# Kernel tuning notes

Hardware: AMD Instinct MI355X
Metric: run time of the kernel (lower is better)

The kernel has to match this reference:

```python
import jax, jax.numpy as jnp
import numpy as np

HIDDEN = 2048
INTERMEDIATE = 8192
NUM_EXPERTS = 8
VOCAB = 100000
EXPERT_INTER = INTERMEDIATE // NUM_EXPERTS  # 1024
B, S = 4, 4096


def setup_inputs() -> dict:
    key = jax.random.key(0)
    k1, k2, k3, k4, k5 = jax.random.split(key, 5)
    hidden_states = jax.random.normal(k1, (B, S, HIDDEN), dtype=jnp.float32)
    token_ids = jax.random.randint(k2, (B, S), 0, VOCAB, dtype=jnp.int64)
    scale = 0.02
    gate_proj = jax.random.normal(k3, (NUM_EXPERTS, HIDDEN, EXPERT_INTER), dtype=jnp.float32) * scale
    up_proj = jax.random.normal(k4, (NUM_EXPERTS, HIDDEN, EXPERT_INTER), dtype=jnp.float32) * scale
    down_proj = jax.random.normal(k5, (NUM_EXPERTS, EXPERT_INTER, HIDDEN), dtype=jnp.float32) * scale
    return {
        "hidden_states": hidden_states,
        "token_ids": token_ids,
        "gate_proj": gate_proj,
        "up_proj": up_proj,
        "down_proj": down_proj,
    }


def _token_to_expert(token_ids):
    # Buffer in the torch module maps contiguous vocab buckets to experts;
    # remainder tokens go to the last expert.
    tokens_per_expert = VOCAB // NUM_EXPERTS
    ids = jnp.clip(token_ids, 0, VOCAB - 1)
    return jnp.minimum(ids // tokens_per_expert, NUM_EXPERTS - 1)


def reference(hidden_states, token_ids, gate_proj, up_proj, down_proj):
    batch, seq_len, hidden = hidden_states.shape
    expert_ids = _token_to_expert(token_ids).reshape(-1)  # [T]
    x = hidden_states.reshape(-1, hidden)  # [T, H]
    out = jnp.zeros_like(x)
    # Fixed small loop over experts (structurally distinct weight slices).
    # Masked dense compute is mathematically identical to the torch module's
    # sort -> per-expert GEMM -> scatter-back (the permutation cancels).
    for e in range(NUM_EXPERTS):
        mask = (expert_ids == e)[:, None]  # [T, 1]
        g = x @ gate_proj[e]               # [T, I_e]
        u = x @ up_proj[e]                 # [T, I_e]
        y = (jax.nn.silu(g) * u) @ down_proj[e]  # [T, H]
        out = out + jnp.where(mask, y, jnp.zeros((), dtype=y.dtype))
    return out.reshape(batch, seq_len, hidden)
```

## Files before the change

### kernel.cpp

```cpp
#include <hip/hip_runtime.h>
#include <hip/hip_bf16.h>
#include <cstdint>
#include <cstddef>

#define HIDDEN   2048
#define EINTER   1024
#define NEXP     8
#define VOCAB_SZ 100000
#define TOK_PER_EXP (VOCAB_SZ / NEXP)

typedef unsigned short u16;
typedef __attribute__((ext_vector_type(8))) short short8;
typedef __attribute__((ext_vector_type(4))) float floatx4;

__device__ __forceinline__ int expert_of(int id) {
  id = id < 0 ? 0 : (id > VOCAB_SZ - 1 ? VOCAB_SZ - 1 : id);
  int e = id / TOK_PER_EXP;
  return e > NEXP - 1 ? NEXP - 1 : e;
}

__device__ __forceinline__ void gl16(const u16* g, u16* l) {
  __builtin_amdgcn_global_load_lds(
      (const __attribute__((address_space(1))) uint32_t*)g,
      (__attribute__((address_space(3))) uint32_t*)l, 16, 0, 0);
}

__device__ __forceinline__ short8 ldfrag(const u16* base, int row, int chunk) {
  return *(const short8*)(base + (row << 6) + (((chunk ^ (row & 7))) << 3));
}

__global__ void count_kernel(const int* __restrict__ tok_ids, int* __restrict__ counts, int T) {
  int t = blockIdx.x * blockDim.x + threadIdx.x;
  if (t < T) atomicAdd(&counts[expert_of(tok_ids[t])], 1);
}

__global__ void scan_kernel(const int* __restrict__ counts, int* __restrict__ offsets,
                            int* __restrict__ cursors) {
  if (threadIdx.x == 0) {
    int s = 0;
    for (int e = 0; e < NEXP; ++e) { offsets[e] = s; cursors[e] = s; s += counts[e]; }
  }
}

__global__ void scatter_kernel(const int* __restrict__ tok_ids, int* __restrict__ cursors,
                               int* __restrict__ tok_list, int T) {
  int t = blockIdx.x * blockDim.x + threadIdx.x;
  if (t < T) {
    int e = expert_of(tok_ids[t]);
    int pos = atomicAdd(&cursors[e], 1);
    tok_list[pos] = t;
  }
}

__global__ void gather_x_kernel(const float* __restrict__ x, const int* __restrict__ tok_list,
                                u16* __restrict__ xp) {
  const int row = blockIdx.x;
  const int tok = tok_list[row];
  const float* src = x + (size_t)tok * HIDDEN;
  u16* dst = xp + (size_t)row * HIDDEN;
  const int k = threadIdx.x * 8;
  float4 a = *(const float4*)(src + k);
  float4 b = *(const float4*)(src + k + 4);
  union { uint4 u; u16 s[8]; } pk;
  const float f[8] = {a.x, a.y, a.z, a.w, b.x, b.y, b.z, b.w};
#pragma unroll
  for (int i = 0; i < 8; ++i) {
    __hip_bfloat16 h = __float2bfloat16(f[i]);
    pk.s[i] = *reinterpret_cast<u16*>(&h);
  }
  *(uint4*)(dst + k) = pk.u;
}

__global__ void transpose_cvt64(const float* __restrict__ in0, u16* __restrict__ out0,
                                const float* __restrict__ in1, u16* __restrict__ out1,
                                int R, int C, int split) {
  __shared__ float ts[64][65];
  const int z = blockIdx.z;
  const bool first = (z < split) || (in1 == nullptr);
  const float* in = first ? in0 : in1;
  u16* outp = first ? out0 : out1;
  const int e = first ? z : z - split;
  const size_t bo = (size_t)e * R * C;
  const int c0 = blockIdx.x * 64, r0 = blockIdx.y * 64;
  const int lr = threadIdx.x >> 2, lq = threadIdx.x & 3;
#pragma unroll
  for (int j = 0; j < 4; ++j)
    *(float4*)&ts[lr][lq * 16 + j * 4] =
        *(const float4*)&in[bo + (size_t)(r0 + lr) * C + c0 + lq * 16 + j * 4];
  __syncthreads();
#pragma unroll
  for (int j = 0; j < 2; ++j) {
    union { uint4 u; u16 s[8]; } pk;
#pragma unroll
    for (int i = 0; i < 8; ++i) {
      __hip_bfloat16 h = __float2bfloat16(ts[lq * 16 + j * 8 + i][lr]);
      pk.s[i] = *reinterpret_cast<u16*>(&h);
    }
    *(uint4*)&outp[bo + (size_t)(c0 + lr) * R + r0 + lq * 16 + j * 8] = pk.u;
  }
}

__global__ __launch_bounds__(256, 2) void gate_up_mfma(
    const u16* __restrict__ xp, const u16* __restrict__ Gt, const u16* __restrict__ Ut,
    const int* __restrict__ counts, const int* __restrict__ offsets,
    u16* __restrict__ act) {
  __shared__ __align__(16) u16 As[128 * 64];
  __shared__ __align__(16) u16 Bg[64 * 64];
  __shared__ __align__(16) u16 Bu[64 * 64];

  const int e = blockIdx.z;
  const int cnt = counts[e];
  const int row0 = blockIdx.y * 128;
  if (row0 >= cnt) return;
  const int off = offsets[e];
  const int i0 = blockIdx.x * 64;

  const int tid  = threadIdx.x;
  const int lane = tid & 63;
  const int wave = tid >> 6;
  const int quad = lane >> 4;
  const int l16  = lane & 15;

  const int lrow   = lane >> 3;
  const int lchunk = (lane & 7) ^ lrow;

  const int wrow = (wave & 1) * 64;
  const int wcol = (wave >> 1) * 32;

  const u16* aptr[4];
#pragma unroll
  for (int it = 0; it < 4; ++it) {
    int r = ((wave + 4 * it) << 3) + lrow;
    int rg = row0 + r; rg = rg < cnt ? rg : cnt - 1;
    aptr[it] = xp + (size_t)(off + rg) * HIDDEN + (lchunk << 3);
  }
  const u16* gptr[2];
  const u16* uptr[2];
#pragma unroll
  for (int it = 0; it < 2; ++it) {
    int n = ((wave + 4 * it) << 3) + lrow;
    gptr[it] = Gt + ((size_t)e * EINTER + i0 + n) * HIDDEN + (lchunk << 3);
    uptr[it] = Ut + ((size_t)e * EINTER + i0 + n) * HIDDEN + (lchunk << 3);
  }

  floatx4 accg[4][2], accu[4][2];
#pragma unroll
  for (int mf = 0; mf < 4; ++mf)
#pragma unroll
    for (int nf = 0; nf < 2; ++nf) {
      floatx4 z = {0.f, 0.f, 0.f, 0.f};
      accg[mf][nf] = z; accu[mf][nf] = z;
    }

  for (int k0 = 0; k0 < HIDDEN; k0 += 64) {
#pragma unroll
    for (int it = 0; it < 4; ++it)
      gl16(aptr[it] + k0, &As[(wave + 4 * it) << 9]);
#pragma unroll
    for (int it = 0; it < 2; ++it) {
      gl16(gptr[it] + k0, &Bg[(wave + 4 * it) << 9]);
      gl16(uptr[it] + k0, &Bu[(wave + 4 * it) << 9]);
    }
    __syncthreads();
#pragma unroll
    for (int s = 0; s < 2; ++s) {
      short8 af[4], bgf[2], buf2[2];
#pragma unroll
      for (int mf = 0; mf < 4; ++mf)
        af[mf] = ldfrag(As, wrow + mf * 16 + l16, s * 4 + quad);
#pragma unroll
      for (int nf = 0; nf < 2; ++nf) {
        bgf[nf]  = ldfrag(Bg, wcol + nf * 16 + l16, s * 4 + quad);
        buf2[nf] = ldfrag(Bu, wcol + nf * 16 + l16, s * 4 + quad);
      }
#pragma unroll
      for (int mf = 0; mf < 4; ++mf)
#pragma unroll
        for (int nf = 0; nf < 2; ++nf) {
          accg[mf][nf] = __builtin_amdgcn_mfma_f32_16x16x32_bf16(af[mf], bgf[nf],  accg[mf][nf], 0, 0, 0);
          accu[mf][nf] = __builtin_amdgcn_mfma_f32_16x16x32_bf16(af[mf], buf2[nf], accu[mf][nf], 0, 0, 0);
        }
    }
    __syncthreads();
  }

#pragma unroll
  for (int mf = 0; mf < 4; ++mf)
#pragma unroll
    for (int nf = 0; nf < 2; ++nf)
#pragma unroll
      for (int rg = 0; rg < 4; ++rg) {
        int r = wrow + mf * 16 + quad * 4 + rg;
        if (row0 + r < cnt) {
          float g = accg[mf][nf][rg];
          float u = accu[mf][nf][rg];
          float y = (g / (1.f + __expf(-g))) * u;
          __hip_bfloat16 h = __float2bfloat16(y);
          act[((size_t)(off + row0 + r)) * EINTER + i0 + wcol + nf * 16 + l16] =
              *reinterpret_cast<u16*>(&h);
        }
      }
}

__global__ __launch_bounds__(256, 2) void down_mfma(
    const u16* __restrict__ act, const u16* __restrict__ Dt,
    const int* __restrict__ counts, const int* __restrict__ offsets,
    const int* __restrict__ tok_list, float* __restrict__ out) {
  __shared__ __align__(16) u16 As[128 * 64];
  __shared__ __align__(16) u16 Bs[128 * 64];
  __shared__ int toks[128];

  const int e = blockIdx.z;
  const int cnt = counts[e];
  const int row0 = blockIdx.y * 128;
  if (row0 >= cnt) return;
  const int off = offsets[e];
  const int j0 = blockIdx.x * 128;

  const int tid  = threadIdx.x;
  const int lane = tid & 63;
  const int wave = tid >> 6;
  const int quad = lane >> 4;
  const int l16  = lane & 15;

  const int lrow   = lane >> 3;
  const int lchunk = (lane & 7) ^ lrow;

  const int wrow = (wave & 1) * 64;
  const int wcol = (wave >> 1) * 64;

  if (tid < 128) {
    int r = row0 + tid;
    toks[tid] = tok_list[off + (r < cnt ? r : cnt - 1)];
  }

  const u16* aptr[4];
  const u16* dptr[4];
#pragma unroll
  for (int it = 0; it < 4; ++it) {
    int r = ((wave + 4 * it) << 3) + lrow;
    int rg = row0 + r; rg = rg < cnt ? rg : cnt - 1;
    aptr[it] = act + (size_t)(off + rg) * EINTER + (lchunk << 3);
    dptr[it] = Dt + ((size_t)e * HIDDEN + j0 + r) * EINTER + (lchunk << 3);
  }

  floatx4 acc[4][4];
#pragma unroll
  for (int mf = 0; mf < 4; ++mf)
#pragma unroll
    for (int nf = 0; nf < 4; ++nf) {
      floatx4 z = {0.f, 0.f, 0.f, 0.f};
      acc[mf][nf] = z;
    }

  for (int k0 = 0; k0 < EINTER; k0 += 64) {
#pragma unroll
    for (int it = 0; it < 4; ++it) {
      gl16(aptr[it] + k0, &As[(wave + 4 * it) << 9]);
      gl16(dptr[it] + k0, &Bs[(wave + 4 * it) << 9]);
    }
    __syncthreads();
#pragma unroll
    for (int s = 0; s < 2; ++s) {
      short8 af[4], bf[4];
#pragma unroll
      for (int mf = 0; mf < 4; ++mf)
        af[mf] = ldfrag(As, wrow + mf * 16 + l16, s * 4 + quad);
#pragma unroll
      for (int nf = 0; nf < 4; ++nf)
        bf[nf] = ldfrag(Bs, wcol + nf * 16 + l16, s * 4 + quad);
#pragma unroll
      for (int mf = 0; mf < 4; ++mf)
#pragma unroll
        for (int nf = 0; nf < 4; ++nf)
          acc[mf][nf] = __builtin_amdgcn_mfma_f32_16x16x32_bf16(af[mf], bf[nf], acc[mf][nf], 0, 0, 0);
    }
    __syncthreads();
  }

#pragma unroll
  for (int mf = 0; mf < 4; ++mf)
#pragma unroll
    for (int nf = 0; nf < 4; ++nf)
#pragma unroll
      for (int rg = 0; rg < 4; ++rg) {
        int r = wrow + mf * 16 + quad * 4 + rg;
        if (row0 + r < cnt)
          out[(size_t)toks[r] * HIDDEN + j0 + wcol + nf * 16 + l16] = acc[mf][nf][rg];
      }
}

#define TM 64
#define TN 64
#define TK 16

__global__ __launch_bounds__(256, 2) void gate_up_fp32(
    const float* __restrict__ x, const float* __restrict__ G, const float* __restrict__ U,
    const int* __restrict__ counts, const int* __restrict__ offsets,
    const int* __restrict__ tok_list, float* __restrict__ act) {
  __shared__ __align__(16) float Xs[TK][TM + 4];
  __shared__ __align__(16) float Gs[TK][TN];
  __shared__ __align__(16) float Us[TK][TN];
  __shared__ int toks[TM];
  const int e = blockIdx.z, cnt = counts[e], row0 = blockIdx.y * TM;
  if (row0 >= cnt) return;
  const int off = offsets[e], i0 = blockIdx.x * TN, tid = threadIdx.x;
  if (tid < TM) { int r = row0 + tid; toks[tid] = tok_list[off + (r < cnt ? r : 0)]; }
  __syncthreads();
  const float* Ge = G + (size_t)e * HIDDEN * EINTER + i0;
  const float* Ue = U + (size_t)e * HIDDEN * EINTER + i0;
  const int kk_ld = tid & 15, r_ld = tid >> 4, i_ld = tid & 63, k_ld = tid >> 6;
  const int tx = tid & 15, ty = tid >> 4;
  float ag[4][4] = {{0.f}}, au[4][4] = {{0.f}};
  for (int k0 = 0; k0 < HIDDEN; k0 += TK) {
#pragma unroll
    for (int rr = 0; rr < 4; ++rr) {
      int r = r_ld + rr * 16;
      Xs[kk_ld][r] = x[(size_t)toks[r] * HIDDEN + k0 + kk_ld];
    }
#pragma unroll
    for (int kk = 0; kk < 4; ++kk) {
      int k = k_ld + kk * 4;
      Gs[k][i_ld] = Ge[(size_t)(k0 + k) * EINTER + i_ld];
      Us[k][i_ld] = Ue[(size_t)(k0 + k) * EINTER + i_ld];
    }
    __syncthreads();
#pragma unroll
    for (int kk = 0; kk < TK; ++kk) {
      float4 a = *(const float4*)&Xs[kk][ty * 4];
      float4 bg = *(const float4*)&Gs[kk][tx * 4];
      float4 bu = *(const float4*)&Us[kk][tx * 4];
      const float av[4] = {a.x, a.y, a.z, a.w}, bgv[4] = {bg.x, bg.y, bg.z, bg.w},
                  buv[4] = {bu.x, bu.y, bu.z, bu.w};
#pragma unroll
      for (int i = 0; i < 4; ++i)
#pragma unroll
        for (int j = 0; j < 4; ++j) {
          ag[i][j] = fmaf(av[i], bgv[j], ag[i][j]);
          au[i][j] = fmaf(av[i], buv[j], au[i][j]);
        }
    }
    __syncthreads();
  }
#pragma unroll
  for (int i = 0; i < 4; ++i) {
    int r = row0 + ty * 4 + i;
    if (r < cnt) {
      float4 o; float* op = (float*)&o;
#pragma unroll
      for (int j = 0; j < 4; ++j) {
        float g = ag[i][j], u = au[i][j];
        op[j] = (g / (1.0f + expf(-g))) * u;
      }
      *(float4*)&act[(size_t)(off + r) * EINTER + i0 + tx * 4] = o;
    }
  }
}

__global__ __launch_bounds__(256, 2) void down_fp32(
    const float* __restrict__ act, const float* __restrict__ D,
    const int* __restrict__ counts, const int* __restrict__ offsets,
    const int* __restrict__ tok_list, float* __restrict__ out) {
  __shared__ __align__(16) float As[TK][TM + 4];
  __shared__ __align__(16) float Ds[TK][TN];
  __shared__ int toks[TM];
  const int e = blockIdx.z, cnt = counts[e], row0 = blockIdx.y * TM;
  if (row0 >= cnt) return;
  const int off = offsets[e], j0 = blockIdx.x * TN, tid = threadIdx.x;
  if (tid < TM) { int r = row0 + tid; toks[tid] = tok_list[off + (r < cnt ? r : 0)]; }
  const float* De = D + (size_t)e * EINTER * HIDDEN + j0;
  const int kk_ld = tid & 15, r_ld = tid >> 4, i_ld = tid & 63, k_ld = tid >> 6;
  const int tx = tid & 15, ty = tid >> 4;
  float acc[4][4] = {{0.f}};
  for (int k0 = 0; k0 < EINTER; k0 += TK) {
#pragma unroll
    for (int rr = 0; rr < 4; ++rr) {
      int r = r_ld + rr * 16;
      int grow = row0 + r;
      As[kk_ld][r] = act[(size_t)(off + (grow < cnt ? grow : 0)) * EINTER + k0 + kk_ld];
    }
#pragma unroll
    for (int kk = 0; kk < 4; ++kk) {
      int k = k_ld + kk * 4;
      Ds[k][i_ld] = De[(size_t)(k0 + k) * HIDDEN + i_ld];
    }
    __syncthreads();
#pragma unroll
    for (int kk = 0; kk < TK; ++kk) {
      float4 a = *(const float4*)&As[kk][ty * 4];
      float4 b = *(const float4*)&Ds[kk][tx * 4];
      const float av[4] = {a.x, a.y, a.z, a.w}, bv[4] = {b.x, b.y, b.z, b.w};
#pragma unroll
      for (int i = 0; i < 4; ++i)
#pragma unroll
        for (int j = 0; j < 4; ++j)
          acc[i][j] = fmaf(av[i], bv[j], acc[i][j]);
    }
    __syncthreads();
  }
#pragma unroll
  for (int i = 0; i < 4; ++i) {
    int r = row0 + ty * 4 + i;
    if (r < cnt) {
      float4 o = {acc[i][0], acc[i][1], acc[i][2], acc[i][3]};
      *(float4*)&out[(size_t)toks[ty * 4 + i] * HIDDEN + j0 + tx * 4] = o;
    }
  }
}

extern "C" void kernel_launch(void* const* d_in, const int* in_sizes, int n_in,
                              void* d_out, int out_size, void* d_ws, size_t ws_size,
                              hipStream_t stream) {
  const float* x       = (const float*)d_in[0];
  const int*   tok_ids = (const int*)d_in[1];
  const float* G       = (const float*)d_in[2];
  const float* U       = (const float*)d_in[3];
  const float* D       = (const float*)d_in[4];
  float* out = (float*)d_out;

  const int T = in_sizes[0] / HIDDEN;

  int* counts   = (int*)d_ws;
  int* offsets  = counts + NEXP;
  int* cursors  = offsets + NEXP;
  int* tok_list = cursors + NEXP;
  size_t hdr_bytes = (((size_t)(3 * NEXP + T) * sizeof(int)) + 255) & ~(size_t)255;

  hipMemsetAsync(counts, 0, NEXP * sizeof(int), stream);
  count_kernel<<<(T + 255) / 256, 256, 0, stream>>>(tok_ids, counts, T);
  scan_kernel<<<1, 64, 0, stream>>>(counts, offsets, cursors);
  scatter_kernel<<<(T + 255) / 256, 256, 0, stream>>>(tok_ids, cursors, tok_list, T);

  const size_t xp_bytes  = (size_t)T * HIDDEN * 2;
  const size_t w_bytes   = (size_t)NEXP * HIDDEN * EINTER * 2;
  const size_t act_bf16  = (size_t)T * EINTER * 2;
  const size_t need_bf16 = hdr_bytes + xp_bytes + 3 * w_bytes + act_bf16;

  if (ws_size >= need_bf16) {
    char* p = (char*)d_ws + hdr_bytes;
    u16* xp = (u16*)p;   p += xp_bytes;
    u16* Gt = (u16*)p;   p += w_bytes;
    u16* Ut = (u16*)p;   p += w_bytes;
    u16* Dt = (u16*)p;   p += w_bytes;
    u16* act = (u16*)p;

    gather_x_kernel<<<T, 256, 0, stream>>>(x, tok_list, xp);
    transpose_cvt64<<<dim3(EINTER / 64, HIDDEN / 64, 2 * NEXP), 256, 0, stream>>>(
        G, Gt, U, Ut, HIDDEN, EINTER, NEXP);
    transpose_cvt64<<<dim3(HIDDEN / 64, EINTER / 64, NEXP), 256, 0, stream>>>(
        D, Dt, nullptr, nullptr, EINTER, HIDDEN, NEXP);

    dim3 g1(EINTER / 64, (T + 127) / 128, NEXP);
    gate_up_mfma<<<g1, 256, 0, stream>>>(xp, Gt, Ut, counts, offsets, act);
    dim3 g2(HIDDEN / 128, (T + 127) / 128, NEXP);
    down_mfma<<<g2, 256, 0, stream>>>(act, Dt, counts, offsets, tok_list, out);
  } else {
    float* act = (float*)((char*)d_ws + hdr_bytes);
    dim3 g1(EINTER / TN, (T + TM - 1) / TM, NEXP);
    gate_up_fp32<<<g1, 256, 0, stream>>>(x, G, U, counts, offsets, tok_list, act);
    dim3 g2(HIDDEN / TN, (T + TM - 1) / TM, NEXP);
    down_fp32<<<g2, 256, 0, stream>>>(act, D, counts, offsets, tok_list, out);
  }
}
```

Baseline: 746.3 us.

## Rewrite MoE GEMMs as 8-wave double-buffered phased pipelines with larger tiles

Replaces the gate/up and down MFMA kernels with 512-thread versions that use 256-row tiles and wider column tiles. Shared memory is double-buffered, and each K step is split into four phases. In each phase, global-to-LDS loads for the next tile are interleaved with MFMA bursts, using explicit waitcnt, barriers and setprio. The aim is to hide global load latency and raise arithmetic intensity per block. The cost is much larger LDS use, which lowers occupancy, and more partially filled tiles per expert because the row granularity is coarser.

```diff
diff --git a/kernel.cpp b/kernel.cpp
--- a/kernel.cpp
+++ b/kernel.cpp
@@ -100,194 +100,371 @@
   }
 }
 
-__global__ __launch_bounds__(256, 2) void gate_up_mfma(
+
+__global__ __launch_bounds__(512, 2) void gate_up_8ph(
     const u16* __restrict__ xp, const u16* __restrict__ Gt, const u16* __restrict__ Ut,
     const int* __restrict__ counts, const int* __restrict__ offsets,
     u16* __restrict__ act) {
-  __shared__ __align__(16) u16 As[128 * 64];
-  __shared__ __align__(16) u16 Bg[64 * 64];
-  __shared__ __align__(16) u16 Bu[64 * 64];
+  __shared__ __align__(16) u16 As[2][256 * 64];
+  __shared__ __align__(16) u16 Bg[2][128 * 64];
+  __shared__ __align__(16) u16 Bu[2][128 * 64];
 
   const int e = blockIdx.z;
   const int cnt = counts[e];
-  const int row0 = blockIdx.y * 128;
+  const int row0 = blockIdx.y * 256;
   if (row0 >= cnt) return;
   const int off = offsets[e];
-  const int i0 = blockIdx.x * 64;
+  const int i0 = blockIdx.x * 128;
 
   const int tid  = threadIdx.x;
   const int lane = tid & 63;
-  const int wave = tid >> 6;
+  const int w    = tid >> 6;
+  const int wr   = w >> 2;
+  const int wc   = w & 3;
   const int quad = lane >> 4;
   const int l16  = lane & 15;
-
   const int lrow   = lane >> 3;
   const int lchunk = (lane & 7) ^ lrow;
 
-  const int wrow = (wave & 1) * 64;
-  const int wcol = (wave >> 1) * 32;
-
-  const u16* aptr[4];
-#pragma unroll
-  for (int it = 0; it < 4; ++it) {
-    int r = ((wave + 4 * it) << 3) + lrow;
-    int rg = row0 + r; rg = rg < cnt ? rg : cnt - 1;
-    aptr[it] = xp + (size_t)(off + rg) * HIDDEN + (lchunk << 3);
-  }
-  const u16* gptr[2];
-  const u16* uptr[2];
+  const u16* apt[4]; int abase[4];
+  {
+    const int bsel[4] = {w, w + 16, w + 8, w + 24};
+#pragma unroll
+    for (int i = 0; i < 4; ++i) {
+      int batch = bsel[i];
+      int r = batch * 8 + lrow;
+      int rg = row0 + r; rg = rg < cnt ? rg : cnt - 1;
+      apt[i] = xp + (size_t)(off + rg) * HIDDEN + (lchunk << 3);
+      abase[i] = batch << 9;
+    }
+  }
+  const u16 *gpt[2], *upt[2]; int bbase[2];
 #pragma unroll
   for (int it = 0; it < 2; ++it) {
-    int n = ((wave + 4 * it) << 3) + lrow;
-    gptr[it] = Gt + ((size_t)e * EINTER + i0 + n) * HIDDEN + (lchunk << 3);
-    uptr[it] = Ut + ((size_t)e * EINTER + i0 + n) * HIDDEN + (lchunk << 3);
-  }
-
-  floatx4 accg[4][2], accu[4][2];
-#pragma unroll
-  for (int mf = 0; mf < 4; ++mf)
-#pragma unroll
-    for (int nf = 0; nf < 2; ++nf) {
-      floatx4 z = {0.f, 0.f, 0.f, 0.f};
-      accg[mf][nf] = z; accu[mf][nf] = z;
-    }
-
-  for (int k0 = 0; k0 < HIDDEN; k0 += 64) {
-#pragma unroll
-    for (int it = 0; it < 4; ++it)
-      gl16(aptr[it] + k0, &As[(wave + 4 * it) << 9]);
-#pragma unroll
-    for (int it = 0; it < 2; ++it) {
-      gl16(gptr[it] + k0, &Bg[(wave + 4 * it) << 9]);
-      gl16(uptr[it] + k0, &Bu[(wave + 4 * it) << 9]);
-    }
-    __syncthreads();
-#pragma unroll
-    for (int s = 0; s < 2; ++s) {
-      short8 af[4], bgf[2], buf2[2];
-#pragma unroll
-      for (int mf = 0; mf < 4; ++mf)
-        af[mf] = ldfrag(As, wrow + mf * 16 + l16, s * 4 + quad);
+    int batch = w + 8 * it;
+    int n = batch * 8 + lrow;
+    gpt[it] = Gt + ((size_t)e * EINTER + i0 + n) * HIDDEN + (lchunk << 3);
+    upt[it] = Ut + ((size_t)e * EINTER + i0 + n) * HIDDEN + (lchunk << 3);
+    bbase[it] = batch << 9;
+  }
+
+  floatx4 accg[2][4][2], accu[2][4][2];
+#pragma unroll
+  for (int mh = 0; mh < 2; ++mh)
+#pragma unroll
+    for (int mf = 0; mf < 4; ++mf)
 #pragma unroll
       for (int nf = 0; nf < 2; ++nf) {
-        bgf[nf]  = ldfrag(Bg, wcol + nf * 16 + l16, s * 4 + quad);
-        buf2[nf] = ldfrag(Bu, wcol + nf * 16 + l16, s * 4 + quad);
+        floatx4 z = {0.f, 0.f, 0.f, 0.f};
+        accg[mh][mf][nf] = z; accu[mh][mf][nf] = z;
       }
-#pragma unroll
-      for (int mf = 0; mf < 4; ++mf)
-#pragma unroll
-        for (int nf = 0; nf < 2; ++nf) {
-          accg[mf][nf] = __builtin_amdgcn_mfma_f32_16x16x32_bf16(af[mf], bgf[nf],  accg[mf][nf], 0, 0, 0);
-          accu[mf][nf] = __builtin_amdgcn_mfma_f32_16x16x32_bf16(af[mf], buf2[nf], accu[mf][nf], 0, 0, 0);
+
+  gl16(apt[0], As[0] + abase[0]); gl16(apt[1], As[0] + abase[1]);
+  gl16(gpt[0], Bg[0] + bbase[0]); gl16(gpt[1], Bg[0] + bbase[1]);
+  gl16(upt[0], Bu[0] + bbase[0]); gl16(upt[1], Bu[0] + bbase[1]);
+  gl16(apt[2], As[0] + abase[2]); gl16(apt[3], As[0] + abase[3]);
+  asm volatile("s_waitcnt vmcnt(4)" ::: "memory");
+  __builtin_amdgcn_s_barrier();
+
+  const int NT = HIDDEN / 64;
+  for (int t = 0; t < NT; ++t) {
+    const int b  = t & 1;
+    const int kn = (t + 1 < NT) ? (t + 1) * 64 : 0;
+    const u16* Ar = As[b]; const u16* Gr = Bg[b]; const u16* Ur = Bu[b];
+    u16* Aw = As[b ^ 1];   u16* Gw = Bg[b ^ 1];   u16* Uw = Bu[b ^ 1];
+
+    short8 af[4][2], bg[2][2], bu[2][2];
+
+#pragma unroll
+    for (int mf = 0; mf < 4; ++mf)
+#pragma unroll
+      for (int s = 0; s < 2; ++s)
+        af[mf][s] = ldfrag(Ar, wr * 128 + mf * 16 + l16, s * 4 + quad);
+#pragma unroll
+    for (int nf = 0; nf < 2; ++nf)
+#pragma unroll
+      for (int s = 0; s < 2; ++s)
+        bg[nf][s] = ldfrag(Gr, wc * 32 + nf * 16 + l16, s * 4 + quad);
+    gl16(apt[0] + kn, Aw + abase[0]); gl16(apt[1] + kn, Aw + abase[1]);
+    gl16(gpt[0] + kn, Gw + bbase[0]); gl16(gpt[1] + kn, Gw + bbase[1]);
+    asm volatile("s_waitcnt vmcnt(6)" ::: "memory");
+    __builtin_amdgcn_s_barrier();
+    asm volatile("s_waitcnt lgkmcnt(0)" ::: "memory");
+    __builtin_amdgcn_sched_barrier(0);
+    __builtin_amdgcn_s_setprio(1);
+#pragma unroll
+    for (int s = 0; s < 2; ++s)
+#pragma unroll
+      for (int mf = 0; mf < 4; ++mf)
+#pragma unroll
+        for (int nf = 0; nf < 2; ++nf)
+          accg[0][mf][nf] = __builtin_amdgcn_mfma_f32_16x16x32_bf16(af[mf][s], bg[nf][s], accg[0][mf][nf], 0, 0, 0);
+    __builtin_amdgcn_s_setprio(0);
+    __builtin_amdgcn_sched_barrier(0);
+    __builtin_amdgcn_s_barrier();
+
+#pragma unroll
+    for (int nf = 0; nf < 2; ++nf)
+#pragma unroll
+      for (int s = 0; s < 2; ++s)
+        bu[nf][s] = ldfrag(Ur, wc * 32 + nf * 16 + l16, s * 4 + quad);
+    gl16(upt[0] + kn, Uw + bbase[0]); gl16(upt[1] + kn, Uw + bbase[1]);
+    asm volatile("s_waitcnt vmcnt(6)" ::: "memory");
+    __builtin_amdgcn_s_barrier();
+    asm volatile("s_waitcnt lgkmcnt(0)" ::: "memory");
+    __builtin_amdgcn_sched_barrier(0);
+    __builtin_amdgcn_s_setprio(1);
+#pragma unroll
+    for (int s = 0; s < 2; ++s)
+#pragma unroll
+      for (int mf = 0; mf < 4; ++mf)
+#pragma unroll
+        for (int nf = 0; nf < 2; ++nf)
+          accu[0][mf][nf] = __builtin_amdgcn_mfma_f32_16x16x32_bf16(af[mf][s], bu[nf][s], accu[0][mf][nf], 0, 0, 0);
+    __builtin_amdgcn_s_setprio(0);
+    __builtin_amdgcn_sched_barrier(0);
+    __builtin_amdgcn_s_barrier();
+
+#pragma unroll
+    for (int mf = 0; mf < 4; ++mf)
+#pragma unroll
+      for (int s = 0; s < 2; ++s)
+        af[mf][s] = ldfrag(Ar, wr * 128 + 64 + mf * 16 + l16, s * 4 + quad);
+    gl16(apt[2] + kn, Aw + abase[2]); gl16(apt[3] + kn, Aw + abase[3]);
+    __builtin_amdgcn_s_barrier();
+    asm volatile("s_waitcnt lgkmcnt(0)" ::: "memory");
+    __builtin_amdgcn_sched_barrier(0);
+    __builtin_amdgcn_s_setprio(1);
+#pragma unroll
+    for (int s = 0; s < 2; ++s)
+#pragma unroll
+      for (int mf = 0; mf < 4; ++mf)
+#pragma unroll
+        for (int nf = 0; nf < 2; ++nf)
+          accg[1][mf][nf] = __builtin_amdgcn_mfma_f32_16x16x32_bf16(af[mf][s], bg[nf][s], accg[1][mf][nf], 0, 0, 0);
+    __builtin_amdgcn_s_setprio(0);
+    __builtin_amdgcn_sched_barrier(0);
+    __builtin_amdgcn_s_barrier();
+
+    asm volatile("s_waitcnt vmcnt(4)" ::: "memory");
+    __builtin_amdgcn_s_barrier();
+    __builtin_amdgcn_s_setprio(1);
+#pragma unroll
+    for (int s = 0; s < 2; ++s)
+#pragma unroll
+      for (int mf = 0; mf < 4; ++mf)
+#pragma unroll
+        for (int nf = 0; nf < 2; ++nf)
+          accu[1][mf][nf] = __builtin_amdgcn_mfma_f32_16x16x32_bf16(af[mf][s], bu[nf][s], accu[1][mf][nf], 0, 0, 0);
+    __builtin_amdgcn_s_setprio(0);
+    __builtin_amdgcn_sched_barrier(0);
+    __builtin_amdgcn_s_barrier();
+  }
+  asm volatile("s_waitcnt vmcnt(0)" ::: "memory");
+
+#pragma unroll
+  for (int mh = 0; mh < 2; ++mh)
+#pragma unroll
+    for (int mf = 0; mf < 4; ++mf)
+#pragma unroll
+      for (int nf = 0; nf < 2; ++nf)
+#pragma unroll
+        for (int rg = 0; rg < 4; ++rg) {
+          int r = wr * 128 + mh * 64 + mf * 16 + quad * 4 + rg;
+          if (row0 + r < cnt) {
+            float g = accg[mh][mf][nf][rg];
+            float u = accu[mh][mf][nf][rg];
+            float y = (g / (1.f + __expf(-g))) * u;
+            __hip_bfloat16 h = __float2bfloat16(y);
+            act[((size_t)(off + row0 + r)) * EINTER + i0 + wc * 32 + nf * 16 + l16] =
+                *reinterpret_cast<u16*>(&h);
+          }
         }
-    }
-    __syncthreads();
-  }
-
-#pragma unroll
-  for (int mf = 0; mf < 4; ++mf)
-#pragma unroll
-    for (int nf = 0; nf < 2; ++nf)
-#pragma unroll
-      for (int rg = 0; rg < 4; ++rg) {
-        int r = wrow + mf * 16 + quad * 4 + rg;
-        if (row0 + r < cnt) {
-          float g = accg[mf][nf][rg];
-          float u = accu[mf][nf][rg];
-          float y = (g / (1.f + __expf(-g))) * u;
-          __hip_bfloat16 h = __float2bfloat16(y);
-          act[((size_t)(off + row0 + r)) * EINTER + i0 + wcol + nf * 16 + l16] =
-              *reinterpret_cast<u16*>(&h);
-        }
-      }
-}
-
-__global__ __launch_bounds__(256, 2) void down_mfma(
+}
+
+__global__ __launch_bounds__(512, 2) void down_8ph(
     const u16* __restrict__ act, const u16* __restrict__ Dt,
     const int* __restrict__ counts, const int* __restrict__ offsets,
     const int* __restrict__ tok_list, float* __restrict__ out) {
-  __shared__ __align__(16) u16 As[128 * 64];
-  __shared__ __align__(16) u16 Bs[128 * 64];
-  __shared__ int toks[128];
+  __shared__ __align__(16) u16 As[2][256 * 64];
+  __shared__ __align__(16) u16 Bs[2][256 * 64];
+  __shared__ int toks[256];
 
   const int e = blockIdx.z;
   const int cnt = counts[e];
-  const int row0 = blockIdx.y * 128;
+  const int row0 = blockIdx.y * 256;
   if (row0 >= cnt) return;
   const int off = offsets[e];
-  const int j0 = blockIdx.x * 128;
+  const int j0 = blockIdx.x * 256;
 
   const int tid  = threadIdx.x;
   const int lane = tid & 63;
-  const int wave = tid >> 6;
+  const int w    = tid >> 6;
+  const int wr   = w >> 2;
+  const int wc   = w & 3;
   const int quad = lane >> 4;
   const int l16  = lane & 15;
-
   const int lrow   = lane >> 3;
   const int lchunk = (lane & 7) ^ lrow;
 
-  const int wrow = (wave & 1) * 64;
-  const int wcol = (wave >> 1) * 64;
-
-  if (tid < 128) {
+  if (tid < 256) {
     int r = row0 + tid;
     toks[tid] = tok_list[off + (r < cnt ? r : cnt - 1)];
   }
 
-  const u16* aptr[4];
-  const u16* dptr[4];
-#pragma unroll
-  for (int it = 0; it < 4; ++it) {
-    int r = ((wave + 4 * it) << 3) + lrow;
-    int rg = row0 + r; rg = rg < cnt ? rg : cnt - 1;
-    aptr[it] = act + (size_t)(off + rg) * EINTER + (lchunk << 3);
-    dptr[it] = Dt + ((size_t)e * HIDDEN + j0 + r) * EINTER + (lchunk << 3);
-  }
-
-  floatx4 acc[4][4];
-#pragma unroll
-  for (int mf = 0; mf < 4; ++mf)
-#pragma unroll
-    for (int nf = 0; nf < 4; ++nf) {
-      floatx4 z = {0.f, 0.f, 0.f, 0.f};
-      acc[mf][nf] = z;
-    }
-
-  for (int k0 = 0; k0 < EINTER; k0 += 64) {
-#pragma unroll
-    for (int it = 0; it < 4; ++it) {
-      gl16(aptr[it] + k0, &As[(wave + 4 * it) << 9]);
-      gl16(dptr[it] + k0, &Bs[(wave + 4 * it) << 9]);
-    }
-    __syncthreads();
-#pragma unroll
-    for (int s = 0; s < 2; ++s) {
-      short8 af[4], bf[4];
-#pragma unroll
-      for (int mf = 0; mf < 4; ++mf)
-        af[mf] = ldfrag(As, wrow + mf * 16 + l16, s * 4 + quad);
-#pragma unroll
-      for (int nf = 0; nf < 4; ++nf)
-        bf[nf] = ldfrag(Bs, wcol + nf * 16 + l16, s * 4 + quad);
-#pragma unroll
-      for (int mf = 0; mf < 4; ++mf)
-#pragma unroll
-        for (int nf = 0; nf < 4; ++nf)
-          acc[mf][nf] = __builtin_amdgcn_mfma_f32_16x16x32_bf16(af[mf], bf[nf], acc[mf][nf], 0, 0, 0);
-    }
-    __syncthreads();
-  }
-
-#pragma unroll
-  for (int mf = 0; mf < 4; ++mf)
-#pragma unroll
-    for (int nf = 0; nf < 4; ++nf)
-#pragma unroll
-      for (int rg = 0; rg < 4; ++rg) {
-        int r = wrow + mf * 16 + quad * 4 + rg;
-        if (row0 + r < cnt)
-          out[(size_t)toks[r] * HIDDEN + j0 + wcol + nf * 16 + l16] = acc[mf][nf][rg];
-      }
+  const u16* apt[4]; int abase[4];
+  {
+    const int bsel[4] = {w, w + 16, w + 8, w + 24};
+#pragma unroll
+    for (int i = 0; i < 4; ++i) {
+      int batch = bsel[i];
+      int r = batch * 8 + lrow;
+      int rg = row0 + r; rg = rg < cnt ? rg : cnt - 1;
+      apt[i] = act + (size_t)(off + rg) * EINTER + (lchunk << 3);
+      abase[i] = batch << 9;
+    }
+  }
+  const u16* dpt[4]; int dbase[4];
+#pragma unroll
+  for (int i = 0; i < 4; ++i) {
+    int batch = w + 8 * i;
+    int n = j0 + batch * 8 + lrow;
+    dpt[i] = Dt + ((size_t)e * HIDDEN + n) * EINTER + (lchunk << 3);
+    dbase[i] = batch << 9;
+  }
+
+  floatx4 acc[2][2][4][2];
+#pragma unroll
+  for (int mh = 0; mh < 2; ++mh)
+#pragma unroll
+    for (int nh = 0; nh < 2; ++nh)
+#pragma unroll
+      for (int mf = 0; mf < 4; ++mf)
+#pragma unroll
+        for (int nf = 0; nf < 2; ++nf) {
+          floatx4 z = {0.f, 0.f, 0.f, 0.f};
+          acc[mh][nh][mf][nf] = z;
+        }
+
+  asm volatile("s_waitcnt lgkmcnt(0)" ::: "memory");
+  gl16(apt[0], As[0] + abase[0]); gl16(apt[1], As[0] + abase[1]);
+  gl16(dpt[0], Bs[0] + dbase[0]); gl16(dpt[1], Bs[0] + dbase[1]);
+  gl16(dpt[2], Bs[0] + dbase[2]); gl16(dpt[3], Bs[0] + dbase[3]);
+  gl16(apt[2], As[0] + abase[2]); gl16(apt[3], As[0] + abase[3]);
+  asm volatile("s_waitcnt vmcnt(4)" ::: "memory");
+  __builtin_amdgcn_s_barrier();
+
+  const int NT = EINTER / 64;
+  for (int t = 0; t < NT; ++t) {
+    const int b  = t & 1;
+    const int kn = (t + 1 < NT) ? (t + 1) * 64 : 0;
+    const u16* Ar = As[b]; const u16* Br = Bs[b];
+    u16* Aw = As[b ^ 1];   u16* Bw = Bs[b ^ 1];
+
+    short8 af[4][2], b0[2][2], b1[2][2];
+
+#pragma unroll
+    for (int mf = 0; mf < 4; ++mf)
+#pragma unroll
+      for (int s = 0; s < 2; ++s)
+        af[mf][s] = ldfrag(Ar, wr * 128 + mf * 16 + l16, s * 4 + quad);
+#pragma unroll
+    for (int nf = 0; nf < 2; ++nf)
+#pragma unroll
+      for (int s = 0; s < 2; ++s)
+        b0[nf][s] = ldfrag(Br, wc * 32 + nf * 16 + l16, s * 4 + quad);
+    gl16(apt[0] + kn, Aw + abase[0]); gl16(apt[1] + kn, Aw + abase[1]);
+    gl16(dpt[0] + kn, Bw + dbase[0]); gl16(dpt[1] + kn, Bw + dbase[1]);
+    asm volatile("s_waitcnt vmcnt(6)" ::: "memory");
+    __builtin_amdgcn_s_barrier();
+    asm volatile("s_waitcnt lgkmcnt(0)" ::: "memory");
+    __builtin_amdgcn_sched_barrier(0);
+    __builtin_amdgcn_s_setprio(1);
+#pragma unroll
+    for (int s = 0; s < 2; ++s)
+#pragma unroll
+      for (int mf = 0; mf < 4; ++mf)
+#pragma unroll
+        for (int nf = 0; nf < 2; ++nf)
+          acc[0][0][mf][nf] = __builtin_amdgcn_mfma_f32_16x16x32_bf16(af[mf][s], b0[nf][s], acc[0][0][mf][nf], 0, 0, 0);
+    __builtin_amdgcn_s_setprio(0);
+    __builtin_amdgcn_sched_barrier(0);
+    __builtin_amdgcn_s_barrier();
+
+#pragma unroll
+    for (int nf = 0; nf < 2; ++nf)
+#pragma unroll
+      for (int s = 0; s < 2; ++s)
+        b1[nf][s] = ldfrag(Br, 128 + wc * 32 + nf * 16 + l16, s * 4 + quad);
+    gl16(dpt[2] + kn, Bw + dbase[2]); gl16(dpt[3] + kn, Bw + dbase[3]);
+    asm volatile("s_waitcnt vmcnt(6)" ::: "memory");
+    __builtin_amdgcn_s_barrier();
+    asm volatile("s_waitcnt lgkmcnt(0)" ::: "memory");
+    __builtin_amdgcn_sched_barrier(0);
+    __builtin_amdgcn_s_setprio(1);
+#pragma unroll
+    for (int s = 0; s < 2; ++s)
+#pragma unroll
+      for (int mf = 0; mf < 4; ++mf)
+#pragma unroll
+        for (int nf = 0; nf < 2; ++nf)
+          acc[0][1][mf][nf] = __builtin_amdgcn_mfma_f32_16x16x32_bf16(af[mf][s], b1[nf][s], acc[0][1][mf][nf], 0, 0, 0);
+    __builtin_amdgcn_s_setprio(0);
+    __builtin_amdgcn_sched_barrier(0);
+    __builtin_amdgcn_s_barrier();
+
+#pragma unroll
+    for (int mf = 0; mf < 4; ++mf)
+#pragma unroll
+      for (int s = 0; s < 2; ++s)
+        af[mf][s] = ldfrag(Ar, wr * 128 + 64 + mf * 16 + l16, s * 4 + quad);
+    gl16(apt[2] + kn, Aw + abase[2]); gl16(apt[3] + kn, Aw + abase[3]);
+    __builtin_amdgcn_s_barrier();
+    asm volatile("s_waitcnt lgkmcnt(0)" ::: "memory");
+    __builtin_amdgcn_sched_barrier(0);
+    __builtin_amdgcn_s_setprio(1);
+#pragma unroll
+    for (int s = 0; s < 2; ++s)
+#pragma unroll
+      for (int mf = 0; mf < 4; ++mf)
+#pragma unroll
+        for (int nf = 0; nf < 2; ++nf)
+          acc[1][0][mf][nf] = __builtin_amdgcn_mfma_f32_16x16x32_bf16(af[mf][s], b0[nf][s], acc[1][0][mf][nf], 0, 0, 0);
+    __builtin_amdgcn_s_setprio(0);
+    __builtin_amdgcn_sched_barrier(0);
+    __builtin_amdgcn_s_barrier();
+
+    asm volatile("s_waitcnt vmcnt(4)" ::: "memory");
+    __builtin_amdgcn_s_barrier();
+    __builtin_amdgcn_s_setprio(1);
+#pragma unroll
+    for (int s = 0; s < 2; ++s)
+#pragma unroll
+      for (int mf = 0; mf < 4; ++mf)
+#pragma unroll
+        for (int nf = 0; nf < 2; ++nf)
+          acc[1][1][mf][nf] = __builtin_amdgcn_mfma_f32_16x16x32_bf16(af[mf][s], b1[nf][s], acc[1][1][mf][nf], 0, 0, 0);
+    __builtin_amdgcn_s_setprio(0);
+    __builtin_amdgcn_sched_barrier(0);
+    __builtin_amdgcn_s_barrier();
+  }
+  asm volatile("s_waitcnt vmcnt(0)" ::: "memory");
+
+#pragma unroll
+  for (int mh = 0; mh < 2; ++mh)
+#pragma unroll
+    for (int nh = 0; nh < 2; ++nh)
+#pragma unroll
+      for (int mf = 0; mf < 4; ++mf)
+#pragma unroll
+        for (int nf = 0; nf < 2; ++nf)
+#pragma unroll
+          for (int rg = 0; rg < 4; ++rg) {
+            int r = wr * 128 + mh * 64 + mf * 16 + quad * 4 + rg;
+            if (row0 + r < cnt)
+              out[(size_t)toks[r] * HIDDEN + j0 + nh * 128 + wc * 32 + nf * 16 + l16] =
+                  acc[mh][nh][mf][nf][rg];
+          }
 }
 
 #define TM 64
@@ -450,10 +627,10 @@
     transpose_cvt64<<<dim3(HIDDEN / 64, EINTER / 64, NEXP), 256, 0, stream>>>(
         D, Dt, nullptr, nullptr, EINTER, HIDDEN, NEXP);
 
-    dim3 g1(EINTER / 64, (T + 127) / 128, NEXP);
-    gate_up_mfma<<<g1, 256, 0, stream>>>(xp, Gt, Ut, counts, offsets, act);
-    dim3 g2(HIDDEN / 128, (T + 127) / 128, NEXP);
-    down_mfma<<<g2, 256, 0, stream>>>(act, Dt, counts, offsets, tok_list, out);
+    dim3 g1(EINTER / 128, (T + 255) / 256, NEXP);
+    gate_up_8ph<<<g1, 512, 0, stream>>>(xp, Gt, Ut, counts, offsets, act);
+    dim3 g2(HIDDEN / 256, (T + 255) / 256, NEXP);
+    down_8ph<<<g2, 512, 0, stream>>>(act, Dt, counts, offsets, tok_list, out);
   } else {
     float* act = (float*)((char*)d_ws + hdr_bytes);
     dim3 g1(EINTER / TN, (T + TM - 1) / TM, NEXP);
```

After: 796.2 us. 6.7% more time.

## Double-buffer LDS in MoE GEMMs with two-phase split prefetch pipeline

Applied to the files above, without the earlier changes.

Both bf16 MFMA kernels (gate/up and down) now keep two LDS buffers and prefetch the next K tile with global_load_lds while computing the current one. Each K step is split into two half phases, with explicit vmcnt waits, barriers, sched_barrier and raised wave priority around the MFMA bursts. The aim is to hide global-to-LDS latency that the old single-buffer load, sync, compute loop exposed. In exchange, LDS use doubles, which may limit blocks per CU, and correctness now depends on hand-counted waitcnt values.

```diff
diff --git a/kernel.cpp b/kernel.cpp
--- a/kernel.cpp
+++ b/kernel.cpp
@@ -100,13 +100,14 @@
   }
 }
 
-__global__ __launch_bounds__(256, 2) void gate_up_mfma(
+
+__global__ __launch_bounds__(256, 2) void gate_up_2ph(
     const u16* __restrict__ xp, const u16* __restrict__ Gt, const u16* __restrict__ Ut,
     const int* __restrict__ counts, const int* __restrict__ offsets,
     u16* __restrict__ act) {
-  __shared__ __align__(16) u16 As[128 * 64];
-  __shared__ __align__(16) u16 Bg[64 * 64];
-  __shared__ __align__(16) u16 Bu[64 * 64];
+  __shared__ __align__(16) u16 As[2][128 * 64];
+  __shared__ __align__(16) u16 Bg[2][64 * 64];
+  __shared__ __align__(16) u16 Bu[2][64 * 64];
 
   const int e = blockIdx.z;
   const int cnt = counts[e];
@@ -120,27 +121,29 @@
   const int wave = tid >> 6;
   const int quad = lane >> 4;
   const int l16  = lane & 15;
-
   const int lrow   = lane >> 3;
   const int lchunk = (lane & 7) ^ lrow;
 
   const int wrow = (wave & 1) * 64;
   const int wcol = (wave >> 1) * 32;
 
-  const u16* aptr[4];
+  const u16* aptr[4]; int ab[4];
 #pragma unroll
   for (int it = 0; it < 4; ++it) {
-    int r = ((wave + 4 * it) << 3) + lrow;
+    int batch = wave + 4 * it;
+    int r = batch * 8 + lrow;
     int rg = row0 + r; rg = rg < cnt ? rg : cnt - 1;
     aptr[it] = xp + (size_t)(off + rg) * HIDDEN + (lchunk << 3);
-  }
-  const u16* gptr[2];
-  const u16* uptr[2];
+    ab[it] = batch << 9;
+  }
+  const u16 *gptr[2], *uptr[2]; int bb[2];
 #pragma unroll
   for (int it = 0; it < 2; ++it) {
-    int n = ((wave + 4 * it) << 3) + lrow;
+    int batch = wave + 4 * it;
+    int n = batch * 8 + lrow;
     gptr[it] = Gt + ((size_t)e * EINTER + i0 + n) * HIDDEN + (lchunk << 3);
     uptr[it] = Ut + ((size_t)e * EINTER + i0 + n) * HIDDEN + (lchunk << 3);
+    bb[it] = batch << 9;
   }
 
   floatx4 accg[4][2], accu[4][2];
@@ -152,37 +155,74 @@
       accg[mf][nf] = z; accu[mf][nf] = z;
     }
 
-  for (int k0 = 0; k0 < HIDDEN; k0 += 64) {
-#pragma unroll
-    for (int it = 0; it < 4; ++it)
-      gl16(aptr[it] + k0, &As[(wave + 4 * it) << 9]);
-#pragma unroll
-    for (int it = 0; it < 2; ++it) {
-      gl16(gptr[it] + k0, &Bg[(wave + 4 * it) << 9]);
-      gl16(uptr[it] + k0, &Bu[(wave + 4 * it) << 9]);
-    }
-    __syncthreads();
-#pragma unroll
-    for (int s = 0; s < 2; ++s) {
-      short8 af[4], bgf[2], buf2[2];
+#pragma unroll
+  for (int it = 0; it < 4; ++it) gl16(aptr[it], As[0] + ab[it]);
+  gl16(gptr[0], Bg[0] + bb[0]); gl16(gptr[1], Bg[0] + bb[1]);
+  gl16(uptr[0], Bu[0] + bb[0]); gl16(uptr[1], Bu[0] + bb[1]);
+  asm volatile("s_waitcnt vmcnt(2)" ::: "memory");
+  __builtin_amdgcn_s_barrier();
+
+  const int NT = HIDDEN / 64;
+  for (int t = 0; t < NT; ++t) {
+    const int b  = t & 1;
+    const int kn = (t + 1 < NT) ? (t + 1) * 64 : 0;
+    const u16* Ar = As[b]; const u16* Gr = Bg[b]; const u16* Ur = Bu[b];
+    u16* Aw = As[b ^ 1];   u16* Gw = Bg[b ^ 1];   u16* Uw = Bu[b ^ 1];
+
+    short8 af[4][2], bg[2][2], bu[2][2];
+
+#pragma unroll
+    for (int mf = 0; mf < 4; ++mf)
+#pragma unroll
+      for (int s = 0; s < 2; ++s)
+        af[mf][s] = ldfrag(Ar, wrow + mf * 16 + l16, s * 4 + quad);
+#pragma unroll
+    for (int nf = 0; nf < 2; ++nf)
+#pragma unroll
+      for (int s = 0; s < 2; ++s)
+        bg[nf][s] = ldfrag(Gr, wcol + nf * 16 + l16, s * 4 + quad);
+#pragma unroll
+    for (int it = 0; it < 4; ++it) gl16(aptr[it] + kn, Aw + ab[it]);
+    gl16(gptr[0] + kn, Gw + bb[0]); gl16(gptr[1] + kn, Gw + bb[1]);
+    asm volatile("s_waitcnt vmcnt(6)" ::: "memory");
+    __builtin_amdgcn_s_barrier();
+    asm volatile("s_waitcnt lgkmcnt(0)" ::: "memory");
+    __builtin_amdgcn_sched_barrier(0);
+    __builtin_amdgcn_s_setprio(1);
+#pragma unroll
+    for (int s = 0; s < 2; ++s)
 #pragma unroll
       for (int mf = 0; mf < 4; ++mf)
-        af[mf] = ldfrag(As, wrow + mf * 16 + l16, s * 4 + quad);
-#pragma unroll
-      for (int nf = 0; nf < 2; ++nf) {
-        bgf[nf]  = ldfrag(Bg, wcol + nf * 16 + l16, s * 4 + quad);
-        buf2[nf] = ldfrag(Bu, wcol + nf * 16 + l16, s * 4 + quad);
-      }
+#pragma unroll
+        for (int nf = 0; nf < 2; ++nf)
+          accg[mf][nf] = __builtin_amdgcn_mfma_f32_16x16x32_bf16(af[mf][s], bg[nf][s], accg[mf][nf], 0, 0, 0);
+    __builtin_amdgcn_s_setprio(0);
+    __builtin_amdgcn_sched_barrier(0);
+    __builtin_amdgcn_s_barrier();
+
+#pragma unroll
+    for (int nf = 0; nf < 2; ++nf)
+#pragma unroll
+      for (int s = 0; s < 2; ++s)
+        bu[nf][s] = ldfrag(Ur, wcol + nf * 16 + l16, s * 4 + quad);
+    gl16(uptr[0] + kn, Uw + bb[0]); gl16(uptr[1] + kn, Uw + bb[1]);
+    asm volatile("s_waitcnt vmcnt(2)" ::: "memory");
+    __builtin_amdgcn_s_barrier();
+    asm volatile("s_waitcnt lgkmcnt(0)" ::: "memory");
+    __builtin_amdgcn_sched_barrier(0);
+    __builtin_amdgcn_s_setprio(1);
+#pragma unroll
+    for (int s = 0; s < 2; ++s)
 #pragma unroll
       for (int mf = 0; mf < 4; ++mf)
 #pragma unroll
-        for (int nf = 0; nf < 2; ++nf) {
-          accg[mf][nf] = __builtin_amdgcn_mfma_f32_16x16x32_bf16(af[mf], bgf[nf],  accg[mf][nf], 0, 0, 0);
-          accu[mf][nf] = __builtin_amdgcn_mfma_f32_16x16x32_bf16(af[mf], buf2[nf], accu[mf][nf], 0, 0, 0);
-        }
-    }
-    __syncthreads();
-  }
+        for (int nf = 0; nf < 2; ++nf)
+          accu[mf][nf] = __builtin_amdgcn_mfma_f32_16x16x32_bf16(af[mf][s], bu[nf][s], accu[mf][nf], 0, 0, 0);
+    __builtin_amdgcn_s_setprio(0);
+    __builtin_amdgcn_sched_barrier(0);
+    __builtin_amdgcn_s_barrier();
+  }
+  asm volatile("s_waitcnt vmcnt(0)" ::: "memory");
 
 #pragma unroll
   for (int mf = 0; mf < 4; ++mf)
@@ -202,12 +242,12 @@
       }
 }
 
-__global__ __launch_bounds__(256, 2) void down_mfma(
+__global__ __launch_bounds__(256, 2) void down_2ph(
     const u16* __restrict__ act, const u16* __restrict__ Dt,
     const int* __restrict__ counts, const int* __restrict__ offsets,
     const int* __restrict__ tok_list, float* __restrict__ out) {
-  __shared__ __align__(16) u16 As[128 * 64];
-  __shared__ __align__(16) u16 Bs[128 * 64];
+  __shared__ __align__(16) u16 As[2][128 * 64];
+  __shared__ __align__(16) u16 Bs[2][128 * 64];
   __shared__ int toks[128];
 
   const int e = blockIdx.z;
@@ -222,7 +262,6 @@
   const int wave = tid >> 6;
   const int quad = lane >> 4;
   const int l16  = lane & 15;
-
   const int lrow   = lane >> 3;
   const int lchunk = (lane & 7) ^ lrow;
 
@@ -234,14 +273,17 @@
     toks[tid] = tok_list[off + (r < cnt ? r : cnt - 1)];
   }
 
-  const u16* aptr[4];
-  const u16* dptr[4];
+  const u16* aptr[4]; int ab[4];
+  const u16* dptr[4]; int db[4];
 #pragma unroll
   for (int it = 0; it < 4; ++it) {
-    int r = ((wave + 4 * it) << 3) + lrow;
+    int batch = wave + 4 * it;
+    int r = batch * 8 + lrow;
     int rg = row0 + r; rg = rg < cnt ? rg : cnt - 1;
     aptr[it] = act + (size_t)(off + rg) * EINTER + (lchunk << 3);
     dptr[it] = Dt + ((size_t)e * HIDDEN + j0 + r) * EINTER + (lchunk << 3);
+    ab[it] = batch << 9;
+    db[it] = batch << 9;
   }
 
   floatx4 acc[4][4];
@@ -253,30 +295,75 @@
       acc[mf][nf] = z;
     }
 
-  for (int k0 = 0; k0 < EINTER; k0 += 64) {
-#pragma unroll
-    for (int it = 0; it < 4; ++it) {
-      gl16(aptr[it] + k0, &As[(wave + 4 * it) << 9]);
-      gl16(dptr[it] + k0, &Bs[(wave + 4 * it) << 9]);
-    }
-    __syncthreads();
-#pragma unroll
-    for (int s = 0; s < 2; ++s) {
-      short8 af[4], bf[4];
+  asm volatile("s_waitcnt lgkmcnt(0)" ::: "memory");
+#pragma unroll
+  for (int it = 0; it < 4; ++it) gl16(aptr[it], As[0] + ab[it]);
+  gl16(dptr[0], Bs[0] + db[0]); gl16(dptr[2], Bs[0] + db[2]);
+  gl16(dptr[1], Bs[0] + db[1]); gl16(dptr[3], Bs[0] + db[3]);
+  asm volatile("s_waitcnt vmcnt(2)" ::: "memory");
+  __builtin_amdgcn_s_barrier();
+
+  const int NT = EINTER / 64;
+  for (int t = 0; t < NT; ++t) {
+    const int b  = t & 1;
+    const int kn = (t + 1 < NT) ? (t + 1) * 64 : 0;
+    const u16* Ar = As[b]; const u16* Br = Bs[b];
+    u16* Aw = As[b ^ 1];   u16* Bw = Bs[b ^ 1];
+
+    short8 af[4][2], bf[4][2];
+
+#pragma unroll
+    for (int mf = 0; mf < 4; ++mf)
+#pragma unroll
+      for (int s = 0; s < 2; ++s)
+        af[mf][s] = ldfrag(Ar, wrow + mf * 16 + l16, s * 4 + quad);
+#pragma unroll
+    for (int nf = 0; nf < 2; ++nf)
+#pragma unroll
+      for (int s = 0; s < 2; ++s)
+        bf[nf][s] = ldfrag(Br, wcol + nf * 16 + l16, s * 4 + quad);
+#pragma unroll
+    for (int it = 0; it < 4; ++it) gl16(aptr[it] + kn, Aw + ab[it]);
+    gl16(dptr[0] + kn, Bw + db[0]); gl16(dptr[2] + kn, Bw + db[2]);
+    asm volatile("s_waitcnt vmcnt(6)" ::: "memory");
+    __builtin_amdgcn_s_barrier();
+    asm volatile("s_waitcnt lgkmcnt(0)" ::: "memory");
+    __builtin_amdgcn_sched_barrier(0);
+    __builtin_amdgcn_s_setprio(1);
+#pragma unroll
+    for (int s = 0; s < 2; ++s)
 #pragma unroll
       for (int mf = 0; mf < 4; ++mf)
-        af[mf] = ldfrag(As, wrow + mf * 16 + l16, s * 4 + quad);
-#pragma unroll
-      for (int nf = 0; nf < 4; ++nf)
-        bf[nf] = ldfrag(Bs, wcol + nf * 16 + l16, s * 4 + quad);
+#pragma unroll
+        for (int nf = 0; nf < 2; ++nf)
+          acc[mf][nf] = __builtin_amdgcn_mfma_f32_16x16x32_bf16(af[mf][s], bf[nf][s], acc[mf][nf], 0, 0, 0);
+    __builtin_amdgcn_s_setprio(0);
+    __builtin_amdgcn_sched_barrier(0);
+    __builtin_amdgcn_s_barrier();
+
+#pragma unroll
+    for (int nf = 0; nf < 2; ++nf)
+#pragma unroll
+      for (int s = 0; s < 2; ++s)
+        bf[2 + nf][s] = ldfrag(Br, wcol + 32 + nf * 16 + l16, s * 4 + quad);
+    gl16(dptr[1] + kn, Bw + db[1]); gl16(dptr[3] + kn, Bw + db[3]);
+    asm volatile("s_waitcnt vmcnt(2)" ::: "memory");
+    __builtin_amdgcn_s_barrier();
+    asm volatile("s_waitcnt lgkmcnt(0)" ::: "memory");
+    __builtin_amdgcn_sched_barrier(0);
+    __builtin_amdgcn_s_setprio(1);
+#pragma unroll
+    for (int s = 0; s < 2; ++s)
 #pragma unroll
       for (int mf = 0; mf < 4; ++mf)
 #pragma unroll
-        for (int nf = 0; nf < 4; ++nf)
-          acc[mf][nf] = __builtin_amdgcn_mfma_f32_16x16x32_bf16(af[mf], bf[nf], acc[mf][nf], 0, 0, 0);
-    }
-    __syncthreads();
-  }
+        for (int nf = 0; nf < 2; ++nf)
+          acc[mf][2 + nf] = __builtin_amdgcn_mfma_f32_16x16x32_bf16(af[mf][s], bf[2 + nf][s], acc[mf][2 + nf], 0, 0, 0);
+    __builtin_amdgcn_s_setprio(0);
+    __builtin_amdgcn_sched_barrier(0);
+    __builtin_amdgcn_s_barrier();
+  }
+  asm volatile("s_waitcnt vmcnt(0)" ::: "memory");
 
 #pragma unroll
   for (int mf = 0; mf < 4; ++mf)
@@ -451,9 +538,9 @@
         D, Dt, nullptr, nullptr, EINTER, HIDDEN, NEXP);
 
     dim3 g1(EINTER / 64, (T + 127) / 128, NEXP);
-    gate_up_mfma<<<g1, 256, 0, stream>>>(xp, Gt, Ut, counts, offsets, act);
+    gate_up_2ph<<<g1, 256, 0, stream>>>(xp, Gt, Ut, counts, offsets, act);
     dim3 g2(HIDDEN / 128, (T + 127) / 128, NEXP);
-    down_mfma<<<g2, 256, 0, stream>>>(act, Dt, counts, offsets, tok_list, out);
+    down_2ph<<<g2, 256, 0, stream>>>(act, Dt, counts, offsets, tok_list, out);
   } else {
     float* act = (float*)((char*)d_ws + hdr_bytes);
     dim3 g1(EINTER / TN, (T + TM - 1) / TM, NEXP);
```

New measurement: 806.1 us. +8.0%, slower.
